# Kernel tuning notes

Hardware: AMD Instinct MI355X
Metric: run time of the kernel (lower is better)

## Reference

```python
import jax, jax.numpy as jnp
import numpy as np

NH = 12  # num_heads

def setup_inputs() -> dict:
    key = jax.random.key(0)
    ks = jax.random.split(key, 8)
    B, N, C = 8, 1024, 768
    d = C // NH  # head_dim == qk_head_dim (qk_head_dim=None)
    s = 0.02
    return {
        "x": jax.random.normal(ks[0], (B, N, C), jnp.float32),
        "Wq": jax.random.normal(ks[1], (C, NH * d), jnp.float32) * s,
        "Wk": jax.random.normal(ks[2], (C, NH * d), jnp.float32) * s,
        "Wv": jax.random.normal(ks[3], (C, C), jnp.float32) * s,
        "Wproj": jax.random.normal(ks[4], (C, C), jnp.float32) * s,
        "proj_b": jax.random.normal(ks[5], (C,), jnp.float32) * s,
        "attn_bias": jax.random.normal(ks[6], (N, N), jnp.float32) * s,
        "head_bias": jax.random.normal(ks[7], (NH, N, N), jnp.float32) * s,
    }

def reference(x, Wq, Wk, Wv, Wproj, proj_b, attn_bias, head_bias):
    B, N, C = x.shape
    d = C // NH
    scale = d ** -0.5
    # projections: [B,N,C] -> [B,nh,N,d]
    q = jnp.einsum('bnc,ce->bne', x, Wq).reshape(B, N, NH, d).transpose(0, 2, 1, 3)
    k = jnp.einsum('bnc,ce->bne', x, Wk).reshape(B, N, NH, d).transpose(0, 2, 1, 3)
    v = jnp.einsum('bnc,ce->bne', x, Wv).reshape(B, N, NH, d).transpose(0, 2, 1, 3)
    # scaled scores + global bias + per-head bias
    scores = jnp.einsum('bhnd,bhmd->bhnm', q * scale, k)
    scores = scores + attn_bias[None, None] + head_bias[None]
    attn = jax.nn.softmax(scores, axis=-1)  # [B,nh,N,N]
    out = jnp.einsum('bhnm,bhmd->bhnd', attn, v)
    out = out.transpose(0, 2, 1, 3).reshape(B, N, C)
    out = jnp.einsum('bnc,ce->bne', out, Wproj) + proj_b
    return out, attn
```

## Files before the change

kernel.cpp:

```cpp
#include <hip/hip_runtime.h>
#include <hip/hip_bf16.h>
#include <cstddef>

#define B_   8
#define N_   1024
#define C_   768
#define NH_  12
#define HD_  64
#define M_   (B_ * N_)

typedef __attribute__((ext_vector_type(8))) short  short8;
typedef __attribute__((ext_vector_type(4))) float  f32x4;

__device__ __forceinline__ unsigned short f2b(float f) {
    union { float f; unsigned u; } v; v.f = f;
    unsigned u = v.u;
    return (unsigned short)((u + 0x7FFFu + ((u >> 16) & 1u)) >> 16);
}
__device__ __forceinline__ float b2f(unsigned short s) {
    union { unsigned u; float f; } v; v.u = ((unsigned)s) << 16;
    return v.f;
}
__device__ __forceinline__ ushort2 pk2(float a, float b) {
    __hip_bfloat162 t = __float22bfloat162_rn(make_float2(a, b));
    return *(ushort2*)&t;
}

__global__ __launch_bounds__(256) void cast_x_kernel(const float* __restrict__ x,
                                                     unsigned short* __restrict__ xb) {
    const int n4 = M_ * C_ / 4;
    for (int i = blockIdx.x * blockDim.x + threadIdx.x; i < n4; i += gridDim.x * blockDim.x) {
        float4 v = ((const float4*)x)[i];
        ushort2 lo = pk2(v.x, v.y), hi = pk2(v.z, v.w);
        ushort4 o; o.x = lo.x; o.y = lo.y; o.z = hi.x; o.w = hi.y;
        ((ushort4*)xb)[i] = o;
    }
}

__global__ __launch_bounds__(256) void bias_combine_kernel(
    const float* __restrict__ ab, const float* __restrict__ hbias,
    unsigned short* __restrict__ bc) {
    const int total4 = NH_ * N_ * N_ / 4;
    const int qm4 = N_ * N_ / 4;
    for (int i = blockIdx.x * blockDim.x + threadIdx.x; i < total4; i += gridDim.x * blockDim.x) {
        int rem = i % qm4;
        float4 a = ((const float4*)ab)[rem];
        float4 h = ((const float4*)hbias)[i];
        ushort2 lo = pk2(a.x + h.x, a.y + h.y), hi = pk2(a.z + h.z, a.w + h.w);
        ushort4 o; o.x = lo.x; o.y = lo.y; o.z = hi.x; o.w = hi.y;
        ((ushort4*)bc)[i] = o;
    }
}

__global__ __launch_bounds__(256) void transpose_cast_kernel(
    const float* __restrict__ w0, const float* __restrict__ w1,
    const float* __restrict__ w2, const float* __restrict__ w3,
    unsigned short* __restrict__ t0, unsigned short* __restrict__ t1,
    unsigned short* __restrict__ t2, unsigned short* __restrict__ t3) {
    const int z = blockIdx.z;
    const float* src = (z == 0) ? w0 : (z == 1) ? w1 : (z == 2) ? w2 : w3;
    unsigned short* dst = (z == 0) ? t0 : (z == 1) ? t1 : (z == 2) ? t2 : t3;
    __shared__ float tile[32][33];
    const int r0 = blockIdx.y * 32, c0 = blockIdx.x * 32;
    const int tx = threadIdx.x & 31, ty = threadIdx.x >> 5;
    #pragma unroll
    for (int p = 0; p < 4; ++p)
        tile[ty + 8 * p][tx] = src[(size_t)(r0 + ty + 8 * p) * C_ + c0 + tx];
    __syncthreads();
    #pragma unroll
    for (int p = 0; p < 4; ++p)
        dst[(size_t)(c0 + ty + 8 * p) * C_ + r0 + tx] = f2b(tile[tx][ty + 8 * p]);
}

__global__ __launch_bounds__(256) void qkv_gemm(
    const unsigned short* __restrict__ A,
    const unsigned short* __restrict__ W0, const unsigned short* __restrict__ W1,
    const unsigned short* __restrict__ W2,
    unsigned short* __restrict__ o0, unsigned short* __restrict__ o1,
    unsigned short* __restrict__ o2) {
    __shared__ unsigned short As[128][40];
    __shared__ unsigned short Bs[64][40];
    const int z = blockIdx.z;
    const unsigned short* Bt = (z == 0) ? W0 : (z == 1) ? W1 : W2;
    const int tid = threadIdx.x;
    const int wid = tid >> 6, lane = tid & 63;
    const int ln = lane & 15, g = lane >> 4;
    const int wm = wid >> 1, wn = wid & 1;
    const int bm = blockIdx.y * 128, bn = blockIdx.x * 64;

    f32x4 acc[4][2];
    #pragma unroll
    for (int i = 0; i < 4; ++i)
        #pragma unroll
        for (int j = 0; j < 2; ++j) acc[i][j] = (f32x4)0.f;

    for (int k0 = 0; k0 < C_; k0 += 32) {
        #pragma unroll
        for (int p = 0; p < 2; ++p) {
            int idx = tid + p * 256;
            int row = idx >> 2, ch = idx & 3;
            *(int4*)&As[row][ch * 8] =
                *(const int4*)&A[(size_t)(bm + row) * C_ + k0 + ch * 8];
        }
        {
            int n = tid >> 2, ch = tid & 3;
            *(int4*)&Bs[n][ch * 8] =
                *(const int4*)&Bt[(size_t)(bn + n) * C_ + k0 + ch * 8];
        }
        __syncthreads();
        short8 a[4], b[2];
        #pragma unroll
        for (int mt = 0; mt < 4; ++mt)
            a[mt] = *(const short8*)&As[wm * 64 + mt * 16 + ln][g * 8];
        #pragma unroll
        for (int nt = 0; nt < 2; ++nt)
            b[nt] = *(const short8*)&Bs[wn * 32 + nt * 16 + ln][g * 8];
        #pragma unroll
        for (int mt = 0; mt < 4; ++mt)
            #pragma unroll
            for (int nt = 0; nt < 2; ++nt)
                acc[mt][nt] = __builtin_amdgcn_mfma_f32_16x16x32_bf16(
                    a[mt], b[nt], acc[mt][nt], 0, 0, 0);
        __syncthreads();
    }

    unsigned short* outp = (z == 0) ? o0 : (z == 1) ? o1 : o2;
    #pragma unroll
    for (int mt = 0; mt < 4; ++mt) {
        #pragma unroll
        for (int nt = 0; nt < 2; ++nt) {
            f32x4 c = acc[mt][nt];
            int rowb = bm + wm * 64 + mt * 16 + g * 4;
            int col  = bn + wn * 32 + nt * 16 + ln;
            int hh = col >> 6, dd = col & 63;
            if (z < 2) {
                #pragma unroll
                for (int i = 0; i < 4; ++i) {
                    int row = rowb + i;
                    int bb = row >> 10, n = row & 1023;
                    outp[((size_t)(bb * NH_ + hh) * N_ + n) * HD_ + dd] = f2b(c[i]);
                }
            } else {
                int bb = rowb >> 10, n0 = rowb & 1023;
                ushort2 lo = pk2(c[0], c[1]), hi = pk2(c[2], c[3]);
                ushort4 pk; pk.x = lo.x; pk.y = lo.y; pk.z = hi.x; pk.w = hi.y;
                *(ushort4*)&outp[((size_t)(bb * NH_ + hh) * HD_ + dd) * N_ + n0] = pk;
            }
        }
    }
}

__global__ __launch_bounds__(256) void proj_gemm(
    const unsigned short* __restrict__ A, const unsigned short* __restrict__ Bt,
    const float* __restrict__ bias, float* __restrict__ outp) {
    __shared__ unsigned short As[128][40];
    __shared__ unsigned short Bs[64][40];
    const int tid = threadIdx.x;
    const int wid = tid >> 6, lane = tid & 63;
    const int ln = lane & 15, g = lane >> 4;
    const int wm = wid >> 1, wn = wid & 1;
    const int bm = blockIdx.y * 128, bn = blockIdx.x * 64;

    f32x4 acc[4][2];
    #pragma unroll
    for (int i = 0; i < 4; ++i)
        #pragma unroll
        for (int j = 0; j < 2; ++j) acc[i][j] = (f32x4)0.f;

    for (int k0 = 0; k0 < C_; k0 += 32) {
        #pragma unroll
        for (int p = 0; p < 2; ++p) {
            int idx = tid + p * 256;
            int row = idx >> 2, ch = idx & 3;
            *(int4*)&As[row][ch * 8] =
                *(const int4*)&A[(size_t)(bm + row) * C_ + k0 + ch * 8];
        }
        {
            int n = tid >> 2, ch = tid & 3;
            *(int4*)&Bs[n][ch * 8] =
                *(const int4*)&Bt[(size_t)(bn + n) * C_ + k0 + ch * 8];
        }
        __syncthreads();
        short8 a[4], b[2];
        #pragma unroll
        for (int mt = 0; mt < 4; ++mt)
            a[mt] = *(const short8*)&As[wm * 64 + mt * 16 + ln][g * 8];
        #pragma unroll
        for (int nt = 0; nt < 2; ++nt)
            b[nt] = *(const short8*)&Bs[wn * 32 + nt * 16 + ln][g * 8];
        #pragma unroll
        for (int mt = 0; mt < 4; ++mt)
            #pragma unroll
            for (int nt = 0; nt < 2; ++nt)
                acc[mt][nt] = __builtin_amdgcn_mfma_f32_16x16x32_bf16(
                    a[mt], b[nt], acc[mt][nt], 0, 0, 0);
        __syncthreads();
    }

    #pragma unroll
    for (int mt = 0; mt < 4; ++mt) {
        #pragma unroll
        for (int nt = 0; nt < 2; ++nt) {
            f32x4 c = acc[mt][nt];
            int rowb = bm + wm * 64 + mt * 16 + g * 4;
            int col  = bn + wn * 32 + nt * 16 + ln;
            float bb = bias[col];
            #pragma unroll
            for (int i = 0; i < 4; ++i)
                outp[(size_t)(rowb + i) * C_ + col] = c[i] + bb;
        }
    }
}

__global__ __launch_bounds__(512) void attn_fused(
    const unsigned short* __restrict__ qh, const unsigned short* __restrict__ kh,
    const unsigned short* __restrict__ vt,
    const unsigned short* __restrict__ bias_c,
    float* __restrict__ attn_out, unsigned short* __restrict__ hb) {
    __shared__ unsigned short sc[32 * 1024];
    __shared__ float sinv[32];
    const int id = blockIdx.x;
    const int xcd = id & 7;
    const int b = (id >> 3) & 7;
    const int qbh = ((id >> 6) << 3) + xcd;
    const int qb0 = (qbh / NH_) * 32;
    const int h = qbh % NH_;
    const int bh = b * NH_ + h;
    const int tid = threadIdx.x;
    const int wid = tid >> 6, lane = tid & 63;
    const int ln = lane & 15, g = lane >> 4;

    #define SCP(row, m) ((unsigned short*)((char*)sc + (row) * 2048 + \
                         (((m) * 2) ^ (((row) & 7) << 4))))

    {
        short8 qf[2][2];
        #pragma unroll
        for (int Mt = 0; Mt < 2; ++Mt)
            #pragma unroll
            for (int kc = 0; kc < 2; ++kc)
                qf[Mt][kc] = *(const short8*)&qh[
                    ((size_t)bh * N_ + qb0 + Mt * 16 + ln) * HD_ + kc * 32 + g * 8];
        const int mb = wid * 128;
        const unsigned short* kbase = kh + (size_t)bh * N_ * HD_;
        short8 k0 = *(const short8*)&kbase[(size_t)(mb + ln) * HD_ + g * 8];
        short8 k1 = *(const short8*)&kbase[(size_t)(mb + ln) * HD_ + 32 + g * 8];
        for (int mt = 0; mt < 8; ++mt) {
            const int m0 = mb + mt * 16;
            const int m1 = (mt < 7) ? m0 + 16 : m0;
            short8 n0 = *(const short8*)&kbase[(size_t)(m1 + ln) * HD_ + g * 8];
            short8 n1 = *(const short8*)&kbase[(size_t)(m1 + ln) * HD_ + 32 + g * 8];
            #pragma unroll
            for (int Mt = 0; Mt < 2; ++Mt) {
                f32x4 s = (f32x4)0.f;
                s = __builtin_amdgcn_mfma_f32_16x16x32_bf16(k0, qf[Mt][0], s, 0, 0, 0);
                s = __builtin_amdgcn_mfma_f32_16x16x32_bf16(k1, qf[Mt][1], s, 0, 0, 0);
                const int mrow = m0 + g * 4;
                ushort2 lo = pk2(s[0] * 0.125f, s[1] * 0.125f);
                ushort2 hi = pk2(s[2] * 0.125f, s[3] * 0.125f);
                ushort4 pk; pk.x = lo.x; pk.y = lo.y; pk.z = hi.x; pk.w = hi.y;
                *(ushort4*)SCP(Mt * 16 + ln, mrow) = pk;
            }
            k0 = n0; k1 = n1;
        }
    }
    __syncthreads();

    {
        const int r = tid >> 4, t16 = tid & 15;
        const unsigned short* brow = bias_c + ((size_t)h * N_ + qb0 + r) * N_;
        f32x4 sv[16];
        float mx = -1e30f;
        #pragma unroll
        for (int j = 0; j < 16; ++j) {
            ushort4 er = *(const ushort4*)SCP(r, t16 * 4 + j * 64);
            ushort4 bb = *(const ushort4*)&brow[t16 * 4 + j * 64];
            sv[j][0] = b2f(er.x) + b2f(bb.x);
            sv[j][1] = b2f(er.y) + b2f(bb.y);
            sv[j][2] = b2f(er.z) + b2f(bb.z);
            sv[j][3] = b2f(er.w) + b2f(bb.w);
            mx = fmaxf(fmaxf(fmaxf(mx, sv[j][0]), fmaxf(sv[j][1], sv[j][2])), sv[j][3]);
        }
        #pragma unroll
        for (int off = 8; off; off >>= 1) mx = fmaxf(mx, __shfl_xor(mx, off, 16));
        float sum = 0.f;
        #pragma unroll
        for (int j = 0; j < 16; ++j) {
            float e0 = __expf(sv[j][0] - mx);
            float e1 = __expf(sv[j][1] - mx);
            float e2 = __expf(sv[j][2] - mx);
            float e3 = __expf(sv[j][3] - mx);
            sv[j][0] = e0; sv[j][1] = e1; sv[j][2] = e2; sv[j][3] = e3;
            sum += (e0 + e1) + (e2 + e3);
            ushort2 lo = pk2(e0, e1), hi = pk2(e2, e3);
            ushort4 pk; pk.x = lo.x; pk.y = lo.y; pk.z = hi.x; pk.w = hi.y;
            *(ushort4*)SCP(r, t16 * 4 + j * 64) = pk;
        }
        #pragma unroll
        for (int off = 8; off; off >>= 1) sum += __shfl_xor(sum, off, 16);
        const float inv = 1.f / sum;
        if (t16 == 0) sinv[r] = inv;
        float* arow = attn_out + ((size_t)bh * N_ + qb0 + r) * N_;
        #pragma unroll
        for (int j = 0; j < 16; ++j) {
            f32x4 o;
            o[0] = sv[j][0] * inv; o[1] = sv[j][1] * inv;
            o[2] = sv[j][2] * inv; o[3] = sv[j][3] * inv;
            __builtin_nontemporal_store(o, (f32x4*)&arow[t16 * 4 + j * 64]);
        }
    }
    __syncthreads();

    {
        const int Mt = wid >> 2, nt = wid & 3;
        const unsigned short* vrow = vt + ((size_t)bh * HD_ + nt * 16 + ln) * N_;
        f32x4 acc = (f32x4)0.f;
        short8 pa = *(const short8*)SCP(Mt * 16 + ln, g * 8);
        short8 vb = *(const short8*)&vrow[g * 8];
        for (int kt = 0; kt < 32; ++kt) {
            const int knext = (kt < 31) ? kt + 1 : kt;
            short8 npa = *(const short8*)SCP(Mt * 16 + ln, knext * 32 + g * 8);
            short8 nvb = *(const short8*)&vrow[knext * 32 + g * 8];
            acc = __builtin_amdgcn_mfma_f32_16x16x32_bf16(pa, vb, acc, 0, 0, 0);
            pa = npa; vb = nvb;
        }
        #pragma unroll
        for (int i = 0; i < 4; ++i) {
            int q = qb0 + Mt * 16 + g * 4 + i;
            float o = acc[i] * sinv[Mt * 16 + g * 4 + i];
            hb[(size_t)((b << 10) + q) * C_ + h * HD_ + nt * 16 + ln] = f2b(o);
        }
    }
    #undef SCP
}

extern "C" void kernel_launch(void* const* d_in, const int* in_sizes, int n_in,
                              void* d_out, int out_size, void* d_ws, size_t ws_size,
                              hipStream_t stream) {
    const float* x         = (const float*)d_in[0];
    const float* Wq        = (const float*)d_in[1];
    const float* Wk        = (const float*)d_in[2];
    const float* Wv        = (const float*)d_in[3];
    const float* Wproj     = (const float*)d_in[4];
    const float* proj_b    = (const float*)d_in[5];
    const float* attn_bias = (const float*)d_in[6];
    const float* head_bias = (const float*)d_in[7];

    float* out  = (float*)d_out;
    float* attn = out + (size_t)B_ * N_ * C_;

    unsigned short* ws = (unsigned short*)d_ws;
    const size_t SZ_X = (size_t)M_ * C_;
    const size_t SZ_W = (size_t)C_ * C_;
    unsigned short* xb  = ws;
    unsigned short* wqt = xb + SZ_X;
    unsigned short* wkt = wqt + SZ_W;
    unsigned short* wvt = wkt + SZ_W;
    unsigned short* wpt = wvt + SZ_W;
    unsigned short* qh  = wpt + SZ_W;
    unsigned short* khd = qh + SZ_X;
    unsigned short* vtp = khd + SZ_X;
    unsigned short* bc  = vtp + SZ_X;
    unsigned short* hb  = xb;

    cast_x_kernel<<<2048, 256, 0, stream>>>(x, xb);
    bias_combine_kernel<<<2048, 256, 0, stream>>>(attn_bias, head_bias, bc);
    transpose_cast_kernel<<<dim3(24, 24, 4), 256, 0, stream>>>(
        Wq, Wk, Wv, Wproj, wqt, wkt, wvt, wpt);

    qkv_gemm<<<dim3(C_ / 64, M_ / 128, 3), 256, 0, stream>>>(
        xb, wqt, wkt, wvt, qh, khd, vtp);

    attn_fused<<<dim3(B_ * (N_ / 32) * NH_), 512, 0, stream>>>(
        qh, khd, vtp, bc, attn, hb);

    proj_gemm<<<dim3(C_ / 64, M_ / 128), 256, 0, stream>>>(hb, wpt, proj_b, out);
}
```

Baseline: 306.4 us.

## Use direct global-to-LDS loads and 128x128 tiles in QKV and projection GEMMs

Both GEMM kernels now load tiles with the global_load_lds builtin, which writes global memory straight into shared memory without a register round trip. The padded LDS layout is dropped for unpadded 32-wide rows. The N tile grows from 64 to 128, so each wave computes a 64x64 output. This raises MFMA work per loaded byte and halves the grid, but the unpadded layout may cause LDS bank conflicts on fragment reads and there is still no double buffering.

```diff
diff --git a/kernel.cpp b/kernel.cpp
--- a/kernel.cpp
+++ b/kernel.cpp
@@ -24,6 +24,11 @@
 __device__ __forceinline__ ushort2 pk2(float a, float b) {
     __hip_bfloat162 t = __float22bfloat162_rn(make_float2(a, b));
     return *(ushort2*)&t;
+}
+__device__ __forceinline__ void gld16(const unsigned short* g, unsigned short* l) {
+    __builtin_amdgcn_global_load_lds(
+        (const __attribute__((address_space(1))) void*)g,
+        (__attribute__((address_space(3))) void*)l, 16, 0, 0);
 }
 
 __global__ __launch_bounds__(256) void cast_x_kernel(const float* __restrict__ x,
@@ -78,47 +83,42 @@
     const unsigned short* __restrict__ W2,
     unsigned short* __restrict__ o0, unsigned short* __restrict__ o1,
     unsigned short* __restrict__ o2) {
-    __shared__ unsigned short As[128][40];
-    __shared__ unsigned short Bs[64][40];
+    __shared__ unsigned short As[128 * 32];
+    __shared__ unsigned short Bs[128 * 32];
     const int z = blockIdx.z;
     const unsigned short* Bt = (z == 0) ? W0 : (z == 1) ? W1 : W2;
     const int tid = threadIdx.x;
     const int wid = tid >> 6, lane = tid & 63;
     const int ln = lane & 15, g = lane >> 4;
     const int wm = wid >> 1, wn = wid & 1;
-    const int bm = blockIdx.y * 128, bn = blockIdx.x * 64;
-
-    f32x4 acc[4][2];
+    const int bm = blockIdx.y * 128, bn = blockIdx.x * 128;
+    const int lrow = lane >> 2, lch = (lane & 3) * 8;
+
+    f32x4 acc[4][4];
     #pragma unroll
     for (int i = 0; i < 4; ++i)
         #pragma unroll
-        for (int j = 0; j < 2; ++j) acc[i][j] = (f32x4)0.f;
+        for (int j = 0; j < 4; ++j) acc[i][j] = (f32x4)0.f;
 
     for (int k0 = 0; k0 < C_; k0 += 32) {
         #pragma unroll
         for (int p = 0; p < 2; ++p) {
-            int idx = tid + p * 256;
-            int row = idx >> 2, ch = idx & 3;
-            *(int4*)&As[row][ch * 8] =
-                *(const int4*)&A[(size_t)(bm + row) * C_ + k0 + ch * 8];
-        }
-        {
-            int n = tid >> 2, ch = tid & 3;
-            *(int4*)&Bs[n][ch * 8] =
-                *(const int4*)&Bt[(size_t)(bn + n) * C_ + k0 + ch * 8];
+            const int rowbase = (wid + p * 4) * 16;
+            gld16(&A [(size_t)(bm + rowbase + lrow) * C_ + k0 + lch], &As[rowbase * 32]);
+            gld16(&Bt[(size_t)(bn + rowbase + lrow) * C_ + k0 + lch], &Bs[rowbase * 32]);
         }
         __syncthreads();
-        short8 a[4], b[2];
+        short8 a[4], b[4];
         #pragma unroll
         for (int mt = 0; mt < 4; ++mt)
-            a[mt] = *(const short8*)&As[wm * 64 + mt * 16 + ln][g * 8];
-        #pragma unroll
-        for (int nt = 0; nt < 2; ++nt)
-            b[nt] = *(const short8*)&Bs[wn * 32 + nt * 16 + ln][g * 8];
+            a[mt] = *(const short8*)&As[(wm * 64 + mt * 16 + ln) * 32 + g * 8];
+        #pragma unroll
+        for (int nt = 0; nt < 4; ++nt)
+            b[nt] = *(const short8*)&Bs[(wn * 64 + nt * 16 + ln) * 32 + g * 8];
         #pragma unroll
         for (int mt = 0; mt < 4; ++mt)
             #pragma unroll
-            for (int nt = 0; nt < 2; ++nt)
+            for (int nt = 0; nt < 4; ++nt)
                 acc[mt][nt] = __builtin_amdgcn_mfma_f32_16x16x32_bf16(
                     a[mt], b[nt], acc[mt][nt], 0, 0, 0);
         __syncthreads();
@@ -128,10 +128,10 @@
     #pragma unroll
     for (int mt = 0; mt < 4; ++mt) {
         #pragma unroll
-        for (int nt = 0; nt < 2; ++nt) {
+        for (int nt = 0; nt < 4; ++nt) {
             f32x4 c = acc[mt][nt];
             int rowb = bm + wm * 64 + mt * 16 + g * 4;
-            int col  = bn + wn * 32 + nt * 16 + ln;
+            int col  = bn + wn * 64 + nt * 16 + ln;
             int hh = col >> 6, dd = col & 63;
             if (z < 2) {
                 #pragma unroll
@@ -153,45 +153,40 @@
 __global__ __launch_bounds__(256) void proj_gemm(
     const unsigned short* __restrict__ A, const unsigned short* __restrict__ Bt,
     const float* __restrict__ bias, float* __restrict__ outp) {
-    __shared__ unsigned short As[128][40];
-    __shared__ unsigned short Bs[64][40];
+    __shared__ unsigned short As[128 * 32];
+    __shared__ unsigned short Bs[128 * 32];
     const int tid = threadIdx.x;
     const int wid = tid >> 6, lane = tid & 63;
     const int ln = lane & 15, g = lane >> 4;
     const int wm = wid >> 1, wn = wid & 1;
-    const int bm = blockIdx.y * 128, bn = blockIdx.x * 64;
-
-    f32x4 acc[4][2];
+    const int bm = blockIdx.y * 128, bn = blockIdx.x * 128;
+    const int lrow = lane >> 2, lch = (lane & 3) * 8;
+
+    f32x4 acc[4][4];
     #pragma unroll
     for (int i = 0; i < 4; ++i)
         #pragma unroll
-        for (int j = 0; j < 2; ++j) acc[i][j] = (f32x4)0.f;
+        for (int j = 0; j < 4; ++j) acc[i][j] = (f32x4)0.f;
 
     for (int k0 = 0; k0 < C_; k0 += 32) {
         #pragma unroll
         for (int p = 0; p < 2; ++p) {
-            int idx = tid + p * 256;
-            int row = idx >> 2, ch = idx & 3;
-            *(int4*)&As[row][ch * 8] =
-                *(const int4*)&A[(size_t)(bm + row) * C_ + k0 + ch * 8];
-        }
-        {
-            int n = tid >> 2, ch = tid & 3;
-            *(int4*)&Bs[n][ch * 8] =
-                *(const int4*)&Bt[(size_t)(bn + n) * C_ + k0 + ch * 8];
+            const int rowbase = (wid + p * 4) * 16;
+            gld16(&A [(size_t)(bm + rowbase + lrow) * C_ + k0 + lch], &As[rowbase * 32]);
+            gld16(&Bt[(size_t)(bn + rowbase + lrow) * C_ + k0 + lch], &Bs[rowbase * 32]);
         }
         __syncthreads();
-        short8 a[4], b[2];
+        short8 a[4], b[4];
         #pragma unroll
         for (int mt = 0; mt < 4; ++mt)
-            a[mt] = *(const short8*)&As[wm * 64 + mt * 16 + ln][g * 8];
-        #pragma unroll
-        for (int nt = 0; nt < 2; ++nt)
-            b[nt] = *(const short8*)&Bs[wn * 32 + nt * 16 + ln][g * 8];
+            a[mt] = *(const short8*)&As[(wm * 64 + mt * 16 + ln) * 32 + g * 8];
+        #pragma unroll
+        for (int nt = 0; nt < 4; ++nt)
+            b[nt] = *(const short8*)&Bs[(wn * 64 + nt * 16 + ln) * 32 + g * 8];
         #pragma unroll
         for (int mt = 0; mt < 4; ++mt)
             #pragma unroll
-            for (int nt = 0; nt < 2; ++nt)
+            for (int nt = 0; nt < 4; ++nt)
                 acc[mt][nt] = __builtin_amdgcn_mfma_f32_16x16x32_bf16(
                     a[mt], b[nt], acc[mt][nt], 0, 0, 0);
         __syncthreads();
@@ -200,10 +195,10 @@
     #pragma unroll
     for (int mt = 0; mt < 4; ++mt) {
         #pragma unroll
-        for (int nt = 0; nt < 2; ++nt) {
+        for (int nt = 0; nt < 4; ++nt) {
             f32x4 c = acc[mt][nt];
             int rowb = bm + wm * 64 + mt * 16 + g * 4;
-            int col  = bn + wn * 32 + nt * 16 + ln;
+            int col  = bn + wn * 64 + nt * 16 + ln;
             float bb = bias[col];
             #pragma unroll
             for (int i = 0; i < 4; ++i)
@@ -368,11 +363,11 @@
     transpose_cast_kernel<<<dim3(24, 24, 4), 256, 0, stream>>>(
         Wq, Wk, Wv, Wproj, wqt, wkt, wvt, wpt);
 
-    qkv_gemm<<<dim3(C_ / 64, M_ / 128, 3), 256, 0, stream>>>(
+    qkv_gemm<<<dim3(C_ / 128, M_ / 128, 3), 256, 0, stream>>>(
         xb, wqt, wkt, wvt, qh, khd, vtp);
 
     attn_fused<<<dim3(B_ * (N_ / 32) * NH_), 512, 0, stream>>>(
         qh, khd, vtp, bc, attn, hb);
 
-    proj_gemm<<<dim3(C_ / 64, M_ / 128), 256, 0, stream>>>(hb, wpt, proj_b, out);
-}
+    proj_gemm<<<dim3(C_ / 128, M_ / 128), 256, 0, stream>>>(hb, wpt, proj_b, out);
+}
```

After: 299.0 us. 2.4% less time.
